# Optimization experiments

Measured on AMD Instinct MI355X. Metric: run time of the kernel, lower is better.

The kernel has to match this reference:

```python
import jax, jax.numpy as jnp
import numpy as np

N = 50000      # number of nodes (rows of edge_embeddings)
E = 800000     # number of edges
D = 256        # edge_dim
TOPK = 50


def setup_inputs() -> dict:
    key = jax.random.key(0)
    k1, k2, k3, k4, k5, k6 = jax.random.split(key, 6)
    edge_embeddings = jax.random.normal(k1, (N, D), dtype=jnp.float32)
    edge_index = jax.random.randint(k2, (2, E), 0, N, dtype=jnp.int64)
    # PyTorch nn.Linear default init: U(-1/sqrt(fan_in), 1/sqrt(fan_in))
    s1 = 1.0 / np.sqrt(2 * D)
    s2 = 1.0 / np.sqrt(D)
    W1 = jax.random.uniform(k3, (2 * D, D), jnp.float32, -s1, s1)
    b1 = jax.random.uniform(k4, (D,), jnp.float32, -s1, s1)
    W2 = jax.random.uniform(k5, (D, 1), jnp.float32, -s2, s2)
    b2 = jax.random.uniform(k6, (1,), jnp.float32, -s2, s2)
    return {"edge_embeddings": edge_embeddings, "W1": W1, "b1": b1,
            "W2": W2, "b2": b2, "edge_index": edge_index, "top_k": TOPK}


def reference(edge_embeddings, W1, b1, W2, b2, edge_index, top_k):
    src, dst = edge_index[0], edge_index[1]           # [E]
    valid = src < dst                                  # original keeps only i<j pairs
    # gather + concat: [E, 2D]
    pair_emb = jnp.concatenate([edge_embeddings[src], edge_embeddings[dst]], axis=-1)
    h = jax.nn.relu(pair_emb @ W1 + b1)                # [E, D]
    score = jax.nn.sigmoid(h @ W2 + b2)[:, 0]          # [E], in (0,1)
    # invalid edges get score -1 (< any sigmoid output) so topk picks only valid ones
    masked = jnp.where(valid, score, jnp.float32(-1.0))
    top_scores, top_idx = jax.lax.top_k(masked, top_k)
    top_pairs = edge_index[:, top_idx]                 # [2, k] (src,dst) of top edges
    return top_pairs, top_scores
```

## Files before the change

kernel.cpp:

```cpp
#include <hip/hip_runtime.h>
#include <hip/hip_bf16.h>
#include <cstdint>

#define TOPK 50
#define CANDS 400
#define HIST_BINS 16384
#define CAND_CAP 16384
#define NFBLK 512
#define SORT_CAP 8192

typedef __attribute__((ext_vector_type(8))) short bf16x8;
typedef __attribute__((ext_vector_type(4))) float f32x4;

__device__ __forceinline__ unsigned short f2bf(float f) {
    unsigned u = __float_as_uint(f);
    u += 0x7FFFu + ((u >> 16) & 1u);
    return (unsigned short)(u >> 16);
}

__global__ __launch_bounds__(256) void prep_kernel(const float* __restrict__ W1,
                                                   unsigned* __restrict__ Wcf4,
                                                   unsigned* __restrict__ hist,
                                                   unsigned* __restrict__ misc,
                                                   const int* __restrict__ eidx) {
    int g = blockIdx.x * blockDim.x + threadIdx.x;
    {
        int l = g & 63;
        int kt = (g >> 6) & 7;
        int nt = g >> 9;
        int col = nt * 16 + (l & 15);
        int kb = kt * 32 + (l >> 4) * 8;
        unsigned short h[8];
#pragma unroll
        for (int j = 0; j < 8; ++j) {
            int k = kb + j;
            float f = (col < 256) ? W1[k * 256 + col] : W1[(256 + k) * 256 + (col - 256)];
            h[j] = f2bf(f);
        }
        unsigned* dst = Wcf4 + (size_t)g * 4;
        dst[0] = (unsigned)h[0] | ((unsigned)h[1] << 16);
        dst[1] = (unsigned)h[2] | ((unsigned)h[3] << 16);
        dst[2] = (unsigned)h[4] | ((unsigned)h[5] << 16);
        dst[3] = (unsigned)h[6] | ((unsigned)h[7] << 16);
    }
    if (g < HIST_BINS) hist[g] = 0;
    if (g == 0) {
        int allz = 1;
        for (int q = 0; q < 64; ++q)
            if (eidx[2 * q + 1] != 0) { allz = 0; break; }
        misc[0] = (unsigned)allz;
        misc[2] = 0;
        misc[3] = 0;
        misc[4] = 0;
    }
}

__global__ __launch_bounds__(256) void cvt_emb(const float* __restrict__ emb,
                                               unsigned* __restrict__ A8f4, int M) {
    __shared__ float sl[16][260];
    const int mt = blockIdx.x;
    const int t = threadIdx.x;
    {
        int row = t >> 4;
        int c0 = (t & 15) * 16;
        int gr = mt * 16 + row;
        float4 v0, v1, v2, v3;
        if (gr < M) {
            const float* sp = emb + (size_t)gr * 256 + c0;
            v0 = *(const float4*)(sp + 0);
            v1 = *(const float4*)(sp + 4);
            v2 = *(const float4*)(sp + 8);
            v3 = *(const float4*)(sp + 12);
        } else {
            v0 = v1 = v2 = v3 = make_float4(0.f, 0.f, 0.f, 0.f);
        }
        *(float4*)&sl[row][c0 + 0] = v0;
        *(float4*)&sl[row][c0 + 4] = v1;
        *(float4*)&sl[row][c0 + 8] = v2;
        *(float4*)&sl[row][c0 + 12] = v3;
    }
    __syncthreads();
    const int w = t >> 6;
    const int l = t & 63;
    const int r = l & 15;
    const int kb0 = (l >> 4) * 8;
#pragma unroll
    for (int it = 0; it < 2; ++it) {
        int kt = w + it * 4;
        int kb = kt * 32 + kb0;
        unsigned short h[8];
#pragma unroll
        for (int j = 0; j < 8; ++j) h[j] = f2bf(sl[r][kb + j]);
        unsigned* dst = A8f4 + ((size_t)(mt * 8 + kt) * 64 + l) * 4;
        dst[0] = (unsigned)h[0] | ((unsigned)h[1] << 16);
        dst[1] = (unsigned)h[2] | ((unsigned)h[3] << 16);
        dst[2] = (unsigned)h[4] | ((unsigned)h[5] << 16);
        dst[3] = (unsigned)h[6] | ((unsigned)h[7] << 16);
    }
}

__global__ __launch_bounds__(256) void gemm_frag(const bf16x8* __restrict__ A8v,
                                                 const bf16x8* __restrict__ Bv,
                                                 const float* __restrict__ b1,
                                                 unsigned char* __restrict__ C8) {
    const int bm = blockIdx.x;
    const int bn = blockIdx.y;
    const int t = threadIdx.x;
    const int w = t >> 6;
    const int l = t & 63;
    const int wm = w >> 1, wn = w & 1;

    f32x4 acc[4][4];
#pragma unroll
    for (int i = 0; i < 4; ++i)
#pragma unroll
        for (int j = 0; j < 4; ++j) acc[i][j] = (f32x4){0.f, 0.f, 0.f, 0.f};

    const int MT0 = bm * 8 + wm * 4;
    const int NT0 = bn * 8 + wn * 4;
#pragma unroll
    for (int kt = 0; kt < 8; ++kt) {
        bf16x8 af[4], bf_[4];
#pragma unroll
        for (int i = 0; i < 4; ++i) af[i] = A8v[(size_t)((MT0 + i) * 8 + kt) * 64 + l];
#pragma unroll
        for (int j = 0; j < 4; ++j) bf_[j] = Bv[(size_t)((NT0 + j) * 8 + kt) * 64 + l];
#pragma unroll
        for (int i = 0; i < 4; ++i)
#pragma unroll
            for (int j = 0; j < 4; ++j)
                acc[i][j] = __builtin_amdgcn_mfma_f32_16x16x32_bf16(af[i], bf_[j], acc[i][j], 0, 0, 0);
    }

    const int row0 = bm * 128 + wm * 64 + (l >> 4) * 4;
    const int col0 = bn * 128 + wn * 64 + (l & 15);
#pragma unroll
    for (int i = 0; i < 4; ++i) {
#pragma unroll
        for (int j = 0; j < 4; ++j) {
            int col = col0 + j * 16;
            float bias = (col < 256) ? b1[col] : 0.f;
#pragma unroll
            for (int r = 0; r < 4; ++r) {
                int row = row0 + i * 16 + r;
                float v = acc[i][j][r] + bias;
                int pk = __builtin_amdgcn_cvt_pk_fp8_f32(v, v, 0, false);
                C8[(size_t)row * 512 + col] = (unsigned char)(pk & 0xFF);
            }
        }
    }
}

__global__ __launch_bounds__(256) void count_valid(const int* __restrict__ eidx,
                                                   const unsigned* __restrict__ misc,
                                                   unsigned* __restrict__ bcount, int E) {
    const int is64 = (int)misc[0];
    const int chunk = (E + gridDim.x - 1) / gridDim.x;
    const int lo = blockIdx.x * chunk;
    const int hi = min(E, lo + chunk);
    unsigned cnt = 0;
    for (int e = lo + threadIdx.x; e < hi; e += blockDim.x) {
        int s, d;
        if (is64) {
            s = ((const int2*)eidx)[e].x;
            d = ((const int2*)eidx)[(size_t)e + E].x;
        } else {
            s = eidx[e];
            d = eidx[e + E];
        }
        cnt += (s < d);
    }
#pragma unroll
    for (int off = 32; off; off >>= 1) cnt += __shfl_xor(cnt, off, 64);
    __shared__ unsigned wsum[4];
    if ((threadIdx.x & 63) == 0) wsum[threadIdx.x >> 6] = cnt;
    __syncthreads();
    if (threadIdx.x == 0)
        bcount[blockIdx.x] = wsum[0] + wsum[1] + wsum[2] + wsum[3];
}

__global__ __launch_bounds__(256) void scan_blocks(const unsigned* __restrict__ bcount,
                                                   unsigned* __restrict__ boffset,
                                                   unsigned* __restrict__ misc) {
    __shared__ unsigned sc[256];
    const int t = threadIdx.x;
    unsigned a = bcount[2 * t], b = bcount[2 * t + 1];
    sc[t] = a + b;
    __syncthreads();
    for (int off = 1; off < 256; off <<= 1) {
        unsigned v = (t >= off) ? sc[t - off] : 0u;
        __syncthreads();
        sc[t] += v;
        __syncthreads();
    }
    unsigned excl = sc[t] - (a + b);
    boffset[2 * t] = excl;
    boffset[2 * t + 1] = excl + a;
    if (t == 255) misc[4] = sc[255];
}

__global__ __launch_bounds__(256) void write_valid(const int* __restrict__ eidx,
                                                   const unsigned* __restrict__ misc,
                                                   const unsigned* __restrict__ boffset,
                                                   int* __restrict__ vsrc,
                                                   int* __restrict__ vdst,
                                                   int* __restrict__ vid, int E) {
    const int is64 = (int)misc[0];
    const int chunk = (E + gridDim.x - 1) / gridDim.x;
    const int lo = blockIdx.x * chunk;
    const int hi = min(E, lo + chunk);
    const int lane = threadIdx.x & 63;
    const int w = threadIdx.x >> 6;
    __shared__ unsigned wcnt[4];
    unsigned running = boffset[blockIdx.x];
    for (int base = lo; base < hi; base += blockDim.x) {
        int e = base + threadIdx.x;
        bool valid = false;
        int s = 0, d = 0;
        if (e < hi) {
            if (is64) {
                s = ((const int2*)eidx)[e].x;
                d = ((const int2*)eidx)[(size_t)e + E].x;
            } else {
                s = eidx[e];
                d = eidx[e + E];
            }
            valid = s < d;
        }
        unsigned long long m = __ballot(valid);
        unsigned pfx = __popcll(m & ((1ull << lane) - 1ull));
        if (lane == 0) wcnt[w] = __popcll(m);
        __syncthreads();
        unsigned wbase = running;
        for (int i = 0; i < w; ++i) wbase += wcnt[i];
        if (valid) {
            unsigned p = wbase + pfx;
            vsrc[p] = s;
            vdst[p] = d;
            vid[p] = e;
        }
        unsigned tot = wcnt[0] + wcnt[1] + wcnt[2] + wcnt[3];
        __syncthreads();
        running += tot;
    }
}

__device__ __forceinline__ float dotq(unsigned a, unsigned b, float4 w) {
    float s;
    s  = fmaxf(__builtin_amdgcn_cvt_f32_fp8(a, 0) + __builtin_amdgcn_cvt_f32_fp8(b, 0), 0.f) * w.x;
    s += fmaxf(__builtin_amdgcn_cvt_f32_fp8(a, 1) + __builtin_amdgcn_cvt_f32_fp8(b, 1), 0.f) * w.y;
    s += fmaxf(__builtin_amdgcn_cvt_f32_fp8(a, 2) + __builtin_amdgcn_cvt_f32_fp8(b, 2), 0.f) * w.z;
    s += fmaxf(__builtin_amdgcn_cvt_f32_fp8(a, 3) + __builtin_amdgcn_cvt_f32_fp8(b, 3), 0.f) * w.w;
    return s;
}

__global__ __launch_bounds__(256) void edge_score_fp8(const unsigned char* __restrict__ C8,
                                                      const int* __restrict__ vsrc,
                                                      const int* __restrict__ vdst,
                                                      const float* __restrict__ W2,
                                                      const float* __restrict__ b2,
                                                      float* __restrict__ svals,
                                                      const unsigned* __restrict__ misc) {
    const int V = (int)misc[4];
    const int lane = threadIdx.x & 63;
    const int q = lane & 15;
    const int g = lane >> 4;
    const int wid = blockIdx.x * (blockDim.x >> 6) + (threadIdx.x >> 6);
    const int nw = gridDim.x * (blockDim.x >> 6);

    const float4 w0 = *(const float4*)&W2[q * 16 + 0];
    const float4 w1 = *(const float4*)&W2[q * 16 + 4];
    const float4 w2 = *(const float4*)&W2[q * 16 + 8];
    const float4 w3 = *(const float4*)&W2[q * 16 + 12];
    const float bb2 = b2[0];

    for (int base = wid * 4; base < V; base += nw * 4) {
        const int slot = base + g;
        const bool ok = slot < V;
        const int src = ok ? vsrc[slot] : 0;
        const int dst = ok ? vdst[slot] : 0;
        const uint4 ua = *(const uint4*)(C8 + (size_t)src * 512 + q * 16);
        const uint4 ub = *(const uint4*)(C8 + (size_t)dst * 512 + 256 + q * 16);
        float p = dotq(ua.x, ub.x, w0);
        p += dotq(ua.y, ub.y, w1);
        p += dotq(ua.z, ub.z, w2);
        p += dotq(ua.w, ub.w, w3);
        p += __shfl_xor(p, 1, 64);
        p += __shfl_xor(p, 2, 64);
        p += __shfl_xor(p, 4, 64);
        p += __shfl_xor(p, 8, 64);
        if (q == 0 && ok) {
            float z = p + bb2;
            float sc = 1.0f / (1.0f + expf(-z));
            svals[slot] = sc;
        }
    }
}

__global__ __launch_bounds__(256) void hist_kernel(const float* __restrict__ svals,
                                                   const unsigned* __restrict__ misc,
                                                   unsigned* __restrict__ hist) {
    __shared__ unsigned lh[HIST_BINS];
    const int V = (int)misc[4];
    const int t = threadIdx.x;
    for (int i = t; i < HIST_BINS; i += 256) lh[i] = 0;
    __syncthreads();
    int i = blockIdx.x * blockDim.x + t;
    int stride = gridDim.x * blockDim.x;
    for (int v = i; v < V; v += stride)
        atomicAdd(&lh[__float_as_uint(svals[v]) >> 16], 1u);
    __syncthreads();
    for (int b = t; b < HIST_BINS; b += 256) {
        unsigned c = lh[b];
        if (c) atomicAdd(&hist[b], c);
    }
}

__global__ void scan_hist(const unsigned* __restrict__ hist, unsigned* __restrict__ misc) {
    __shared__ unsigned chunk[256];
    int t = threadIdx.x;
    unsigned s = 0;
    for (int i = 0; i < 64; ++i) s += hist[t * 64 + i];
    chunk[t] = s;
    __syncthreads();
    if (t == 0) {
        unsigned cum = 0;
        int c;
        unsigned thr = 0;
        for (c = 255; c >= 0; --c) {
            if (cum + chunk[c] >= CANDS) break;
            cum += chunk[c];
        }
        if (c >= 0) {
            for (int b = c * 64 + 63; b >= c * 64; --b) {
                cum += hist[b];
                if (cum >= CANDS) { thr = ((unsigned)b) << 16; break; }
            }
        }
        misc[2] = thr;
    }
}

__global__ void compact(const float* __restrict__ svals, const int* __restrict__ vid,
                        unsigned* __restrict__ misc,
                        unsigned long long* __restrict__ cand) {
    const int V = (int)misc[4];
    const unsigned thr = misc[2];
    int i = blockIdx.x * blockDim.x + threadIdx.x;
    int stride = gridDim.x * blockDim.x;
    for (int v = i; v < V; v += stride) {
        unsigned bits = __float_as_uint(svals[v]);
        if (bits >= thr) {
            unsigned pos = atomicAdd(&misc[3], 1u);
            if (pos < CAND_CAP)
                cand[pos] = ((unsigned long long)bits << 32) |
                            (unsigned)(0xFFFFFFFFu - (unsigned)vid[v]);
        }
    }
}

__global__ __launch_bounds__(256) void rescore(const float* __restrict__ emb,
                                               const float* __restrict__ W1,
                                               const float* __restrict__ b1,
                                               const float* __restrict__ W2,
                                               const float* __restrict__ b2,
                                               const int* __restrict__ eidx,
                                               const unsigned long long* __restrict__ cand,
                                               const unsigned* __restrict__ misc,
                                               unsigned long long* __restrict__ rescored,
                                               int E) {
    __shared__ float es[256], ed[256];
    __shared__ float red[256];
    const int C = (int)min(misc[3], (unsigned)CAND_CAP);
    const int is64 = (int)misc[0];
    const int t = threadIdx.x;
    for (int c = blockIdx.x; c < C; c += gridDim.x) {
        unsigned long long entry = cand[c];
        unsigned e = 0xFFFFFFFFu - (unsigned)(entry & 0xFFFFFFFFu);
        int src, dst;
        if (is64) {
            src = eidx[2 * (size_t)e];
            dst = eidx[2 * ((size_t)e + E)];
        } else {
            src = eidx[e];
            dst = eidx[e + E];
        }
        es[t] = emb[(size_t)src * 256 + t];
        ed[t] = emb[(size_t)dst * 256 + t];
        __syncthreads();
        float h = b1[t];
#pragma unroll 8
        for (int k = 0; k < 256; ++k) h += es[k] * W1[k * 256 + t];
#pragma unroll 8
        for (int k = 0; k < 256; ++k) h += ed[k] * W1[(256 + k) * 256 + t];
        red[t] = fmaxf(h, 0.f) * W2[t];
        __syncthreads();
        for (int s = 128; s; s >>= 1) {
            if (t < s) red[t] += red[t + s];
            __syncthreads();
        }
        if (t == 0) {
            float z = red[0] + b2[0];
            float sc = 1.0f / (1.0f + expf(-z));
            rescored[c] = ((unsigned long long)__float_as_uint(sc) << 32) |
                          (unsigned)(0xFFFFFFFFu - e);
        }
        __syncthreads();
    }
}

__global__ __launch_bounds__(256) void final_topk(unsigned long long* __restrict__ rescored,
                                                  const unsigned* __restrict__ misc,
                                                  const int* __restrict__ eidx,
                                                  float* __restrict__ out, int E) {
    __shared__ unsigned long long a[SORT_CAP];
    const int t = threadIdx.x;
    const int C = (int)min(misc[3], (unsigned)CAND_CAP);
    const int is64 = (int)misc[0];

    if (C <= SORT_CAP) {
        int n = 256;
        while (n < C) n <<= 1;
        for (int i = t; i < n; i += 256) a[i] = (i < C) ? rescored[i] : 0ull;
        __syncthreads();
        for (int k = 2; k <= n; k <<= 1) {
            for (int j = k >> 1; j > 0; j >>= 1) {
                for (int i = t; i < n; i += 256) {
                    int ixj = i ^ j;
                    if (ixj > i) {
                        unsigned long long x = a[i], y = a[ixj];
                        bool sw = ((i & k) == 0) ? (x < y) : (x > y);
                        if (sw) { a[i] = y; a[ixj] = x; }
                    }
                }
                __syncthreads();
            }
        }
        if (t < TOPK) {
            unsigned long long m = a[t];
            if (m != 0ull) {
                unsigned bits = (unsigned)(m >> 32);
                unsigned e = 0xFFFFFFFFu - (unsigned)(m & 0xFFFFFFFFu);
                int src, dst;
                if (is64) {
                    src = eidx[2 * (size_t)e];
                    dst = eidx[2 * ((size_t)e + E)];
                } else {
                    src = eidx[e];
                    dst = eidx[e + E];
                }
                out[t] = (float)src;
                out[TOPK + t] = (float)dst;
                out[2 * TOPK + t] = __uint_as_float(bits);
            } else {
                out[t] = -1.f;
                out[TOPK + t] = -1.f;
                out[2 * TOPK + t] = -1.f;
            }
        }
        return;
    }

    __shared__ unsigned long long red[256];
    for (int r = 0; r < TOPK; ++r) {
        unsigned long long best = 0ull;
        for (int i = t; i < C; i += 256) {
            unsigned long long v = rescored[i];
            if (v > best) best = v;
        }
        red[t] = best;
        __syncthreads();
        for (int s = 128; s; s >>= 1) {
            if (t < s) {
                if (red[t + s] > red[t]) red[t] = red[t + s];
            }
            __syncthreads();
        }
        unsigned long long m = red[0];
        __syncthreads();
        for (int i = t; i < C; i += 256)
            if (rescored[i] == m) rescored[i] = 0ull;
        if (t == 0) {
            if (m != 0ull) {
                unsigned bits = (unsigned)(m >> 32);
                unsigned e = 0xFFFFFFFFu - (unsigned)(m & 0xFFFFFFFFu);
                int src, dst;
                if (is64) {
                    src = eidx[2 * (size_t)e];
                    dst = eidx[2 * ((size_t)e + E)];
                } else {
                    src = eidx[e];
                    dst = eidx[e + E];
                }
                out[r] = (float)src;
                out[TOPK + r] = (float)dst;
                out[2 * TOPK + r] = __uint_as_float(bits);
            } else {
                out[r] = -1.f;
                out[TOPK + r] = -1.f;
                out[2 * TOPK + r] = -1.f;
            }
        }
        __syncthreads();
    }
}

extern "C" void kernel_launch(void* const* d_in, const int* in_sizes, int n_in,
                              void* d_out, int out_size, void* d_ws, size_t ws_size,
                              hipStream_t stream) {
    const float* emb = (const float*)d_in[0];
    const float* W1  = (const float*)d_in[1];
    const float* b1  = (const float*)d_in[2];
    const float* W2  = (const float*)d_in[3];
    const float* b2  = (const float*)d_in[4];
    const int*   eidx = (const int*)d_in[5];

    const int M = in_sizes[0] / 256;
    const int E = in_sizes[5] / 2;
    const int Mpad = ((M + 127) / 128) * 128;

    char* p = (char*)d_ws;
    auto alloc = [&](size_t bytes) {
        char* r = p;
        p += (bytes + 255) & ~(size_t)255;
        return r;
    };
    unsigned* A8f4 = (unsigned*)alloc((size_t)Mpad * 256 * 2);
    unsigned* Wcf4 = (unsigned*)alloc(256 * 512 * 2);
    unsigned char* C8 = (unsigned char*)alloc((size_t)Mpad * 512);
    float* svals = (float*)alloc((size_t)E * 4);
    int* vsrc = (int*)alloc((size_t)E * 4);
    int* vdst = (int*)alloc((size_t)E * 4);
    int* vid  = (int*)alloc((size_t)E * 4);
    unsigned* hist = (unsigned*)alloc(HIST_BINS * 4);
    unsigned long long* cand = (unsigned long long*)alloc(CAND_CAP * 8);
    unsigned long long* resc = (unsigned long long*)alloc(CAND_CAP * 8);
    unsigned* bcount = (unsigned*)alloc(NFBLK * 4);
    unsigned* boffset = (unsigned*)alloc(NFBLK * 4);
    unsigned* misc = (unsigned*)alloc(256);

    float* out = (float*)d_out;

    prep_kernel<<<64, 256, 0, stream>>>(W1, Wcf4, hist, misc, eidx);

    cvt_emb<<<Mpad / 16, 256, 0, stream>>>(emb, A8f4, M);

    dim3 ggrid(Mpad / 128, 4);
    gemm_frag<<<ggrid, 256, 0, stream>>>((const bf16x8*)A8f4, (const bf16x8*)Wcf4, b1, C8);

    count_valid<<<NFBLK, 256, 0, stream>>>(eidx, misc, bcount, E);
    scan_blocks<<<1, 256, 0, stream>>>(bcount, boffset, misc);
    write_valid<<<NFBLK, 256, 0, stream>>>(eidx, misc, boffset, vsrc, vdst, vid, E);

    edge_score_fp8<<<2048, 256, 0, stream>>>(C8, vsrc, vdst, W2, b2, svals, misc);

    hist_kernel<<<128, 256, 0, stream>>>(svals, misc, hist);

    scan_hist<<<1, 256, 0, stream>>>(hist, misc);

    compact<<<1024, 256, 0, stream>>>(svals, vid, misc, cand);

    rescore<<<1024, 256, 0, stream>>>(emb, W1, b1, W2, b2, eidx, cand, misc, resc, E);

    final_topk<<<1, 256, 0, stream>>>(resc, misc, eidx, out, E);
}
```

Measured before the change: 167.2 us.

## Fuse embedding bf16 conversion into node GEMM via swizzled shared-memory fragments

```diff
diff --git a/kernel.cpp b/kernel.cpp
--- a/kernel.cpp
+++ b/kernel.cpp
@@ -55,97 +55,66 @@
     }
 }
 
-__global__ __launch_bounds__(256) void cvt_emb(const float* __restrict__ emb,
-                                               unsigned* __restrict__ A8f4, int M) {
-    __shared__ float sl[16][260];
-    const int mt = blockIdx.x;
-    const int t = threadIdx.x;
-    {
-        int row = t >> 4;
-        int c0 = (t & 15) * 16;
-        int gr = mt * 16 + row;
-        float4 v0, v1, v2, v3;
-        if (gr < M) {
-            const float* sp = emb + (size_t)gr * 256 + c0;
-            v0 = *(const float4*)(sp + 0);
-            v1 = *(const float4*)(sp + 4);
-            v2 = *(const float4*)(sp + 8);
-            v3 = *(const float4*)(sp + 12);
-        } else {
-            v0 = v1 = v2 = v3 = make_float4(0.f, 0.f, 0.f, 0.f);
-        }
-        *(float4*)&sl[row][c0 + 0] = v0;
-        *(float4*)&sl[row][c0 + 4] = v1;
-        *(float4*)&sl[row][c0 + 8] = v2;
-        *(float4*)&sl[row][c0 + 12] = v3;
-    }
-    __syncthreads();
-    const int w = t >> 6;
-    const int l = t & 63;
-    const int r = l & 15;
-    const int kb0 = (l >> 4) * 8;
-#pragma unroll
-    for (int it = 0; it < 2; ++it) {
-        int kt = w + it * 4;
-        int kb = kt * 32 + kb0;
-        unsigned short h[8];
-#pragma unroll
-        for (int j = 0; j < 8; ++j) h[j] = f2bf(sl[r][kb + j]);
-        unsigned* dst = A8f4 + ((size_t)(mt * 8 + kt) * 64 + l) * 4;
-        dst[0] = (unsigned)h[0] | ((unsigned)h[1] << 16);
-        dst[1] = (unsigned)h[2] | ((unsigned)h[3] << 16);
-        dst[2] = (unsigned)h[4] | ((unsigned)h[5] << 16);
-        dst[3] = (unsigned)h[6] | ((unsigned)h[7] << 16);
-    }
-}
-
-__global__ __launch_bounds__(256) void gemm_frag(const bf16x8* __restrict__ A8v,
-                                                 const bf16x8* __restrict__ Bv,
-                                                 const float* __restrict__ b1,
-                                                 unsigned char* __restrict__ C8) {
-    const int bm = blockIdx.x;
-    const int bn = blockIdx.y;
+__global__ __launch_bounds__(256) void gemm_fused(const float* __restrict__ emb,
+                                                  const bf16x8* __restrict__ Bv,
+                                                  const float* __restrict__ b1,
+                                                  unsigned char* __restrict__ C8, int M) {
+    __shared__ uint4 afrag[2048];
     const int t = threadIdx.x;
     const int w = t >> 6;
     const int l = t & 63;
-    const int wm = w >> 1, wn = w & 1;
-
-    f32x4 acc[4][4];
-#pragma unroll
-    for (int i = 0; i < 4; ++i)
-#pragma unroll
-        for (int j = 0; j < 4; ++j) acc[i][j] = (f32x4){0.f, 0.f, 0.f, 0.f};
-
-    const int MT0 = bm * 8 + wm * 4;
-    const int NT0 = bn * 8 + wn * 4;
+
+    uint2* w2 = (uint2*)afrag;
+#pragma unroll
+    for (int iter = 0; iter < 16; ++iter) {
+        int r = iter * 4 + w;
+        int c0 = l * 4;
+        int gr = blockIdx.x * 64 + r;
+        float4 v = make_float4(0.f, 0.f, 0.f, 0.f);
+        if (gr < M) v = *(const float4*)&emb[(size_t)gr * 256 + c0];
+        unsigned u0 = (unsigned)f2bf(v.x) | ((unsigned)f2bf(v.y) << 16);
+        unsigned u1 = (unsigned)f2bf(v.z) | ((unsigned)f2bf(v.w) << 16);
+        int mt = r >> 4;
+        int kt = c0 >> 5;
+        int lane = (r & 15) + ((c0 & 31) >> 3) * 16;
+        int f = mt * 8 + kt;
+        int slot = f * 64 + (lane ^ (f & 7));
+        w2[slot * 2 + ((c0 & 7) >> 2)] = make_uint2(u0, u1);
+    }
+    __syncthreads();
+
+    bf16x8 af[8];
 #pragma unroll
     for (int kt = 0; kt < 8; ++kt) {
-        bf16x8 af[4], bf_[4];
-#pragma unroll
-        for (int i = 0; i < 4; ++i) af[i] = A8v[(size_t)((MT0 + i) * 8 + kt) * 64 + l];
-#pragma unroll
-        for (int j = 0; j < 4; ++j) bf_[j] = Bv[(size_t)((NT0 + j) * 8 + kt) * 64 + l];
-#pragma unroll
-        for (int i = 0; i < 4; ++i)
-#pragma unroll
-            for (int j = 0; j < 4; ++j)
-                acc[i][j] = __builtin_amdgcn_mfma_f32_16x16x32_bf16(af[i], bf_[j], acc[i][j], 0, 0, 0);
-    }
-
-    const int row0 = bm * 128 + wm * 64 + (l >> 4) * 4;
-    const int col0 = bn * 128 + wn * 64 + (l & 15);
-#pragma unroll
-    for (int i = 0; i < 4; ++i) {
-#pragma unroll
-        for (int j = 0; j < 4; ++j) {
-            int col = col0 + j * 16;
+        int f = w * 8 + kt;
+        af[kt] = *(const bf16x8*)&afrag[f * 64 + (l ^ kt)];
+    }
+
+    const int row0 = blockIdx.x * 64 + w * 16 + (l >> 4) * 4;
+#pragma unroll
+    for (int nq = 0; nq < 4; ++nq) {
+        f32x4 acc[8];
+#pragma unroll
+        for (int nt = 0; nt < 8; ++nt) acc[nt] = (f32x4){0.f, 0.f, 0.f, 0.f};
+#pragma unroll
+        for (int kt = 0; kt < 8; ++kt) {
+            bf16x8 bf_[8];
+#pragma unroll
+            for (int nt = 0; nt < 8; ++nt)
+                bf_[nt] = Bv[(size_t)((nq * 8 + nt) * 8 + kt) * 64 + l];
+#pragma unroll
+            for (int nt = 0; nt < 8; ++nt)
+                acc[nt] = __builtin_amdgcn_mfma_f32_16x16x32_bf16(af[kt], bf_[nt], acc[nt], 0, 0, 0);
+        }
+#pragma unroll
+        for (int nt = 0; nt < 8; ++nt) {
+            int col = nq * 128 + nt * 16 + (l & 15);
             float bias = (col < 256) ? b1[col] : 0.f;
 #pragma unroll
             for (int r = 0; r < 4; ++r) {
-                int row = row0 + i * 16 + r;
-                float v = acc[i][j][r] + bias;
+                float v = acc[nt][r] + bias;
                 int pk = __builtin_amdgcn_cvt_pk_fp8_f32(v, v, 0, false);
-                C8[(size_t)row * 512 + col] = (unsigned char)(pk & 0xFF);
+                C8[(size_t)(row0 + r) * 512 + col] = (unsigned char)(pk & 0xFF);
             }
         }
     }
@@ -517,7 +486,7 @@
 
     const int M = in_sizes[0] / 256;
     const int E = in_sizes[5] / 2;
-    const int Mpad = ((M + 127) / 128) * 128;
+    const int Mpad = ((M + 63) / 64) * 64;
 
     char* p = (char*)d_ws;
     auto alloc = [&](size_t bytes) {
@@ -525,7 +494,6 @@
         p += (bytes + 255) & ~(size_t)255;
         return r;
     };
-    unsigned* A8f4 = (unsigned*)alloc((size_t)Mpad * 256 * 2);
     unsigned* Wcf4 = (unsigned*)alloc(256 * 512 * 2);
     unsigned char* C8 = (unsigned char*)alloc((size_t)Mpad * 512);
     float* svals = (float*)alloc((size_t)E * 4);
@@ -543,10 +511,7 @@
 
     prep_kernel<<<64, 256, 0, stream>>>(W1, Wcf4, hist, misc, eidx);
 
-    cvt_emb<<<Mpad / 16, 256, 0, stream>>>(emb, A8f4, M);
-
-    dim3 ggrid(Mpad / 128, 4);
-    gemm_frag<<<ggrid, 256, 0, stream>>>((const bf16x8*)A8f4, (const bf16x8*)Wcf4, b1, C8);
+    gemm_fused<<<Mpad / 64, 256, 0, stream>>>(emb, (const bf16x8*)Wcf4, b1, C8, M);
 
     count_valid<<<NFBLK, 256, 0, stream>>>(eidx, misc, bcount, E);
     scan_blocks<<<1, 256, 0, stream>>>(bcount, boffset, misc);
```

Measured after the change: 166.1 us. Within noise of the previous version (-0.7%).
